# Optimization experiments

Hardware: AMD Instinct MI355X
Metric: run time of the kernel (lower is better)

Reference implementation:

```python
import jax, jax.numpy as jnp
import numpy as np
from jax import lax

EPS = 1e-5
C, H, W, G = 512, 32, 32, 32


def instance_norm(x):
    # torch InstanceNorm2d: affine=False, biased variance over (H,W)
    mu = x.mean(axis=(2, 3), keepdims=True)
    var = ((x - mu) ** 2).mean(axis=(2, 3), keepdims=True)
    return (x - mu) / jnp.sqrt(var + EPS)


def conv2d(x, w, stride=1, padding=0, groups=1, lhs_dilation=None):
    return lax.conv_general_dilated(
        x, w, (stride, stride), [(padding, padding)] * 2,
        lhs_dilation=lhs_dilation, feature_group_count=groups,
        dimension_numbers=('NCHW', 'OIHW', 'NCHW'))


def leaky_relu(x):
    return jnp.where(x >= 0, x, 0.2 * x)


def unfold(img, k, s):
    # img: (C,H,W) -> (nH*nW, C, k, k); matches torch unfold(1,k,s).unfold(2,k,s)
    c, h, w = img.shape
    nH = (h - k) // s + 1
    nW = (w - k) // s + 1
    rows = []
    for i in range(k):
        cols = [img[:, i:i + s * (nH - 1) + 1:s, j:j + s * (nW - 1) + 1:s] for j in range(k)]
        rows.append(jnp.stack(cols, axis=-1))  # (C,nH,nW,k)
    p = jnp.stack(rows, axis=-2)  # (C,nH,nW,k,k)
    return p.transpose(1, 2, 0, 3, 4).reshape(nH * nW, c, k, k)


def ral(bg, fg, rate=2, ksize=3, scale=10.0):
    # Region Affinity Layer (contextual-attention style), batch = 1
    b, c, h, w = fg.shape
    fh, fw = h // rate, w // rate
    # bilinear downsample by exactly 2 (half-pixel) == 2x2 average pooling
    fg_small = fg.reshape(b, c, fh, rate, fw, rate).mean(axis=(3, 5))
    bk = 2 * rate
    bg_patches = unfold(jnp.pad(bg, ((0, 0), (0, 0), (1, 1), (1, 1)))[0], bk, rate)      # (256,C,4,4)
    fg_patches = unfold(jnp.pad(fg_small, ((0, 0), (0, 0), (1, 1), (1, 1)))[0], ksize, 1)  # (256,C,3,3)
    norm = jnp.sqrt((fg_patches ** 2).sum(axis=(1, 2, 3), keepdims=True))
    fgp_n = fg_patches / jnp.maximum(norm, 1e-4)
    score = conv2d(fg_small, fgp_n, padding=1)        # (1,256,16,16)
    attn = jax.nn.softmax(score * scale, axis=1)
    # conv_transpose2d(attn, bg_patches, stride=rate, padding=1) via lhs dilation
    w_t = jnp.flip(bg_patches, axis=(-2, -1)).transpose(1, 0, 2, 3)  # (C,256,4,4)
    return conv2d(attn, w_t, padding=bk - 2, lhs_dilation=(rate, rate)) / 4.0  # (1,C,32,32)


def forward(x, gus, w_sk3, b_sk3, w_sk5, b_sk5, w_sk7, b_sk7,
            w_fc, b_fc, w_fc0, b_fc0, w_fc1, b_fc1, w_fc2, b_fc2, w_down, w_fuse):
    # ---- SKConv (M=3 branches: k=3/5/7, groups=32) ----
    feas = []
    for wgt, bias, pad in ((w_sk3, b_sk3, 1), (w_sk5, b_sk5, 2), (w_sk7, b_sk7, 3)):
        f = conv2d(x, wgt, padding=pad, groups=G) + bias[None, :, None, None]
        feas.append(jax.nn.relu(instance_norm(f)))
    feas = jnp.stack(feas, axis=1)                # (B,3,C,H,W)
    fea_s = feas.sum(axis=1).mean(axis=(2, 3))    # (B,C) global pool
    fea_z = fea_s @ w_fc.T + b_fc                 # (B,32)
    att = jnp.stack([fea_z @ w_fc0.T + b_fc0,
                     fea_z @ w_fc1.T + b_fc1,
                     fea_z @ w_fc2.T + b_fc2], axis=1)  # (B,3,C)
    att = jax.nn.softmax(att, axis=1)[..., None, None]
    out_32 = (feas * att).sum(axis=1)             # (1,C,32,32)
    out_res = out_32
    out_32 = ral(out_32, out_32)
    b, c, h, w = out_32.shape
    # ---- gaussian-weighted broadcast sum: (P,H,W)x(C,H,W)->(P,C)->raw reshape ----
    gus_out = jnp.einsum('pxy,cxy->pc', gus, out_32[0]).reshape(b, c, h, w)
    # ---- CSA patch correlation ----
    csa2_in = jax.nn.sigmoid(out_32)
    p_fff = unfold(jnp.pad(out_32, ((0, 0), (0, 0), (1, 1), (1, 1)))[0], 3, 1)    # (1024,C,3,3)
    p_f = unfold(jnp.pad(csa2_in, ((0, 0), (0, 0), (1, 1), (1, 1)))[0], 3, 1)     # (1024,C,3,3)
    p_conv = unfold(csa2_in[0], 1, 1)                                             # (1024,C,1,1)
    csa_a = (p_conv * p_f).mean(axis=1)                                           # (1024,3,3)
    csa_a = jax.nn.softmax(csa_a.reshape(h * w, 9), axis=1).reshape(h * w, 1, 3, 3)
    out_csa = (csa_a * p_fff).sum(axis=(-2, -1)).reshape(b, c, h, w)
    # ---- fuse ----
    z = jnp.concatenate([gus_out, out_csa], axis=1)       # (1,1024,32,32)
    z = leaky_relu(instance_norm(conv2d(z, w_down)))
    z = jnp.concatenate([z, out_res], axis=1)             # (1,1024,32,32)
    return leaky_relu(instance_norm(conv2d(z, w_fuse)))   # (1,512,32,32)


def _gaussian_buffer():
    # util.gussin(1.5): gaussian centered at every grid position of a 32x32 map
    v = 1.5
    r = np.arange(32)
    i, k, x, y = np.meshgrid(r, r, r, r, indexing='ij')
    g = np.exp(-((x - i) ** 2 + (y - k) ** 2) / (2 * v * v)) / (2 * np.pi * v * v)
    return jnp.asarray(g.reshape(32 * 32, 32, 32), dtype=jnp.float32)


def setup_inputs():
    key = jax.random.key(0)
    ks = jax.random.split(key, 12)
    s = 0.02
    return {
        'x': jax.random.normal(ks[0], (1, C, H, W), jnp.float32),
        'gus': _gaussian_buffer(),
        'w_sk3': jax.random.normal(ks[1], (C, C // G, 3, 3), jnp.float32) * s,
        'b_sk3': jnp.zeros((C,), jnp.float32),
        'w_sk5': jax.random.normal(ks[2], (C, C // G, 5, 5), jnp.float32) * s,
        'b_sk5': jnp.zeros((C,), jnp.float32),
        'w_sk7': jax.random.normal(ks[3], (C, C // G, 7, 7), jnp.float32) * s,
        'b_sk7': jnp.zeros((C,), jnp.float32),
        'w_fc': jax.random.normal(ks[4], (32, C), jnp.float32) * s,
        'b_fc': jnp.zeros((32,), jnp.float32),
        'w_fc0': jax.random.normal(ks[5], (C, 32), jnp.float32) * s,
        'b_fc0': jnp.zeros((C,), jnp.float32),
        'w_fc1': jax.random.normal(ks[6], (C, 32), jnp.float32) * s,
        'b_fc1': jnp.zeros((C,), jnp.float32),
        'w_fc2': jax.random.normal(ks[7], (C, 32), jnp.float32) * s,
        'b_fc2': jnp.zeros((C,), jnp.float32),
        'w_down': jax.random.normal(ks[8], (512, 1024, 1, 1), jnp.float32) * s,
        'w_fuse': jax.random.normal(ks[9], (512, 1024, 1, 1), jnp.float32) * s,
    }


def reference(x, gus, w_sk3, b_sk3, w_sk5, b_sk5, w_sk7, b_sk7, w_fc, b_fc,
              w_fc0, b_fc0, w_fc1, b_fc1, w_fc2, b_fc2, w_down, w_fuse):
    return forward(x, gus, w_sk3, b_sk3, w_sk5, b_sk5, w_sk7, b_sk7,
                   w_fc, b_fc, w_fc0, b_fc0, w_fc1, b_fc1, w_fc2, b_fc2,
                   w_down, w_fuse)
```

## Files before the change

kernel.cpp:

```cpp
#include <hip/hip_runtime.h>
#include <math.h>

#define EPSN 1e-5f

typedef __attribute__((ext_vector_type(8))) short bf16x8;
typedef __attribute__((ext_vector_type(4))) float f32x4;

__device__ __forceinline__ ushort f2bf(float f) {
  unsigned u = __float_as_uint(f);
  unsigned r = (u + 0x7fff + ((u >> 16) & 1)) >> 16;
  return (ushort)r;
}
__device__ __forceinline__ float bf2f(ushort h) {
  return __uint_as_float(((unsigned)h) << 16);
}

__device__ __forceinline__ void breduce2(float& a, float& b, float* lds) {
#pragma unroll
  for (int o = 32; o > 0; o >>= 1) {
    a += __shfl_down(a, o);
    b += __shfl_down(b, o);
  }
  int lane = threadIdx.x & 63, wid = threadIdx.x >> 6;
  __syncthreads();
  if (lane == 0) { lds[wid] = a; lds[4 + wid] = b; }
  __syncthreads();
  a = lds[0] + lds[1] + lds[2] + lds[3];
  b = lds[4] + lds[5] + lds[6] + lds[7];
}

__device__ __forceinline__ float breduce_sum(float v, float* lds) {
#pragma unroll
  for (int o = 32; o > 0; o >>= 1) v += __shfl_down(v, o);
  int lane = threadIdx.x & 63, wid = threadIdx.x >> 6;
  __syncthreads();
  if (lane == 0) lds[wid] = v;
  __syncthreads();
  return lds[0] + lds[1] + lds[2] + lds[3];
}

__device__ __forceinline__ float breduce_max(float v, float* lds) {
#pragma unroll
  for (int o = 32; o > 0; o >>= 1) v = fmaxf(v, __shfl_down(v, o));
  int lane = threadIdx.x & 63, wid = threadIdx.x >> 6;
  __syncthreads();
  if (lane == 0) lds[wid] = v;
  __syncthreads();
  return fmaxf(fmaxf(lds[0], lds[1]), fmaxf(lds[2], lds[3]));
}

__global__ void pre_kernel(const float* __restrict__ gus,
                           const float* __restrict__ wdown,
                           const float* __restrict__ wfuse,
                           const float* __restrict__ w3,
                           const float* __restrict__ w5,
                           const float* __restrict__ w7,
                           ushort* __restrict__ gus_bf,
                           ushort* __restrict__ wdown_bf,
                           ushort* __restrict__ wfuse_bf,
                           ushort* __restrict__ resd,
                           ushort* __restrict__ Apk_g,
                           ushort* __restrict__ Acomb,
                           float* __restrict__ diagsum) {
  int bid = blockIdx.x, tid = threadIdx.x;
  if (bid < 2048) {
    int i = bid * 1024 + tid * 4;
    if (i < 1048576) {
      float4 v = *(const float4*)&gus[i];
      int m = i >> 10, n = i & 1023;
      int y = n >> 5, x = n & 31;
      int idxb = ((y >> 1) << 4) + (x >> 1);
      int py = y & 1;
      ushort2 e0 = {f2bf(v.x), f2bf(v.z)};
      ushort2 e1 = {f2bf(v.y), f2bf(v.w)};
      *(ushort2*)&gus_bf[(size_t)m * 1024 + (py * 2 + 0) * 256 + idxb] = e0;
      *(ushort2*)&gus_bf[(size_t)m * 1024 + (py * 2 + 1) * 256 + idxb] = e1;
    } else {
      const float* src; ushort* dst; int off;
      if (i < 1572864) { src = wdown; dst = wdown_bf; off = i - 1048576; }
      else { src = wfuse; dst = wfuse_bf; off = i - 1572864; }
      float4 v = *(const float4*)&src[off];
      ushort4 o = {f2bf(v.x), f2bf(v.y), f2bf(v.z), f2bf(v.w)};
      *(ushort4*)&dst[off] = o;
    }
  } else if (bid < 2304) {
    int t8 = (bid - 2048) * 256 + tid;
    uint4 z = {0u, 0u, 0u, 0u};
#pragma unroll
    for (int k = 0; k < 4; ++k) *(uint4*)&resd[(size_t)(t8 + k * 65536) * 8] = z;
  } else if (bid < 5056) {
    int i2 = (bid - 2304) * 256 + tid;
    int g = i2 / 22016;
    int r = i2 - g * 22016;
    int p = r >> 9;
    int r5 = r & 511;
    int quad = r5 >> 7, m16 = (r5 >> 3) & 15, j = r & 7;
    int k = quad * 8 + j, tp = k >> 4, ic = k & 15;
    float val = 0.f;
    if (p < 25) {
      int t = 2 * p + tp;
      if (t < 49) val = w7[(size_t)(g * 16 + m16) * 784 + ic * 49 + t];
    } else if (p < 38) {
      int t = 2 * (p - 25) + tp;
      if (t < 25) val = w5[(size_t)(g * 16 + m16) * 400 + ic * 25 + t];
    } else {
      int t = 2 * (p - 38) + tp;
      if (t < 9) val = w3[(size_t)(g * 16 + m16) * 144 + ic * 9 + t];
    }
    Apk_g[i2] = f2bf(val);
  } else if (bid < 5568) {
    int j = (bid - 5056) * 256 + tid;
    uint4 z = {0u, 0u, 0u, 0u};
    ((uint4*)Acomb)[j] = z;
  } else {
    diagsum[tid] = 0.f;
  }
}

__global__ __launch_bounds__(256) void sk_mfma(const float* __restrict__ x,
                                               const ushort* __restrict__ Apk_g,
                                               ushort* __restrict__ feasRawH) {
  __shared__ ushort xg[10 * 38 * 24];
  int bid = blockIdx.x, tid = threadIdx.x;
  int g = bid >> 3, sl = bid & 7, y0 = sl * 4;
  for (int i = tid; i < 4560; i += 256) ((uint*)xg)[i] = 0u;
  __syncthreads();
  for (int i = tid; i < 5120; i += 256) {
    int lr = i >> 9, ic = (i >> 5) & 15, xc = i & 31;
    int y = y0 + lr - 3;
    if ((unsigned)y < 32u)
      xg[(lr * 38 + xc + 3) * 24 + ic] =
          f2bf(x[(size_t)(g * 16 + ic) * 1024 + y * 32 + xc]);
  }
  __syncthreads();
  int wv = tid >> 6, lane = tid & 63, quad = lane >> 4, m16 = lane & 15;
  int qh = (quad & 1) * 8, tp = quad >> 1;
  const ushort* Ag = Apk_g + (size_t)g * 22016;
  f32x4 acc[2][3] = {};
#pragma unroll
  for (int p = 0; p < 25; ++p) {
    bf16x8 af = *(const bf16x8*)&Ag[(p * 4 + quad) * 128 + m16 * 8];
    int t = 2 * p + tp;
    if (t > 48) t = 48;
    int ky = t / 7, kx = t - ky * 7;
#pragma unroll
    for (int ti = 0; ti < 2; ++ti) {
      int T = wv + ti * 4, tl = T >> 1, x0c = (T & 1) * 16;
      bf16x8 bf = *(const bf16x8*)&xg[((tl + ky) * 38 + x0c + m16 + kx) * 24 + qh];
      acc[ti][2] = __builtin_amdgcn_mfma_f32_16x16x32_bf16(af, bf, acc[ti][2], 0, 0, 0);
    }
  }
#pragma unroll
  for (int p = 0; p < 13; ++p) {
    bf16x8 af = *(const bf16x8*)&Ag[((p + 25) * 4 + quad) * 128 + m16 * 8];
    int t = 2 * p + tp;
    if (t > 24) t = 24;
    int ky = t / 5, kx = t - ky * 5;
#pragma unroll
    for (int ti = 0; ti < 2; ++ti) {
      int T = wv + ti * 4, tl = T >> 1, x0c = (T & 1) * 16;
      bf16x8 bf =
          *(const bf16x8*)&xg[((tl + ky + 1) * 38 + x0c + m16 + kx + 1) * 24 + qh];
      acc[ti][1] = __builtin_amdgcn_mfma_f32_16x16x32_bf16(af, bf, acc[ti][1], 0, 0, 0);
    }
  }
#pragma unroll
  for (int p = 0; p < 5; ++p) {
    bf16x8 af = *(const bf16x8*)&Ag[((p + 38) * 4 + quad) * 128 + m16 * 8];
    int t = 2 * p + tp;
    if (t > 8) t = 8;
    int ky = t / 3, kx = t - ky * 3;
#pragma unroll
    for (int ti = 0; ti < 2; ++ti) {
      int T = wv + ti * 4, tl = T >> 1, x0c = (T & 1) * 16;
      bf16x8 bf =
          *(const bf16x8*)&xg[((tl + ky + 2) * 38 + x0c + m16 + kx + 2) * 24 + qh];
      acc[ti][0] = __builtin_amdgcn_mfma_f32_16x16x32_bf16(af, bf, acc[ti][0], 0, 0, 0);
    }
  }
  int cb = g * 16 + quad * 4;
#pragma unroll
  for (int ti = 0; ti < 2; ++ti) {
    int T = wv + ti * 4, tl = T >> 1, x0c = (T & 1) * 16;
    int pos = (y0 + tl) * 32 + x0c + m16;
#pragma unroll
    for (int br = 0; br < 3; ++br)
#pragma unroll
      for (int r = 0; r < 4; ++r)
        feasRawH[(size_t)(br * 512 + cb + r) * 1024 + pos] = f2bf(acc[ti][br][r]);
  }
}

__global__ __launch_bounds__(256) void sk_norm(const ushort* __restrict__ rawH,
                                               ushort* __restrict__ feasH,
                                               float* __restrict__ bmean) {
  __shared__ float red[8];
  int mc = blockIdx.x, tid = threadIdx.x;
  float v[4];
  {
    ushort4 h = *(const ushort4*)&rawH[(size_t)mc * 1024 + tid * 4];
    v[0] = bf2f(h.x); v[1] = bf2f(h.y); v[2] = bf2f(h.z); v[3] = bf2f(h.w);
  }
  float s = 0.f, ss = 0.f;
#pragma unroll
  for (int r = 0; r < 4; ++r) { s += v[r]; ss += v[r] * v[r]; }
  breduce2(s, ss, red);
  float mean = s * (1.f / 1024.f);
  float var = ss * (1.f / 1024.f) - mean * mean;
  float inv = rsqrtf(var + EPSN);
  float rs = 0.f;
  ushort4 o;
#pragma unroll
  for (int r = 0; r < 4; ++r) {
    float t = (v[r] - mean) * inv;
    t = t > 0.f ? t : 0.f;
    ((ushort*)&o)[r] = f2bf(t);
    rs += t;
  }
  *(ushort4*)&feasH[(size_t)mc * 1024 + tid * 4] = o;
  float tot = breduce_sum(rs, red);
  if (tid == 0) bmean[mc] = tot * (1.f / 1024.f);
}

__global__ __launch_bounds__(256) void blend_fc(
    const ushort* __restrict__ feasH, const float* __restrict__ bmean,
    const float* __restrict__ wfc, const float* __restrict__ bfc,
    const float* __restrict__ w0, const float* __restrict__ b0,
    const float* __restrict__ w1, const float* __restrict__ b1,
    const float* __restrict__ w2, const float* __restrict__ b2,
    float* __restrict__ res, ushort* __restrict__ Zt2,
    ushort* __restrict__ resd) {
  __shared__ float sfea[512];
  __shared__ float zpart[8][32];
  __shared__ float zz[32];
  __shared__ float lv[3][32];
  __shared__ float attb[3][32];
  __shared__ float tile[32][33];
  int tid = threadIdx.x;
  int pb = blockIdx.x * 32, cb = blockIdx.y * 32;
  for (int c = tid; c < 512; c += 256)
    sfea[c] = bmean[c] + bmean[512 + c] + bmean[1024 + c];
  __syncthreads();
  {
    int j = tid & 31, seg = tid >> 5;
    float p = 0.f;
    for (int c = seg * 64; c < seg * 64 + 64; ++c) p += sfea[c] * wfc[j * 512 + c];
    zpart[seg][j] = p;
  }
  __syncthreads();
  if (tid < 32) {
    float d = bfc[tid];
#pragma unroll
    for (int s = 0; s < 8; ++s) d += zpart[s][tid];
    zz[tid] = d;
// ... 287 lines not shown
      a[t] = (red9[0][t] + red9[1][t] + red9[2][t] + red9[3][t]) * (1.f / 512.f);
    float mx = a[0];
#pragma unroll
    for (int t = 1; t < 9; ++t) mx = fmaxf(mx, a[t]);
    float sum = 0.f;
#pragma unroll
    for (int t = 0; t < 9; ++t) { a[t] = expf(a[t] - mx); sum += a[t]; }
    float inv = 1.f / sum;
#pragma unroll
    for (int t = 0; t < 9; ++t) a9s[t] = a[t] * inv;
  }
  __syncthreads();
  float2 acc = {0.f, 0.f};
#pragma unroll
  for (int u = 0; u < 3; ++u) {
    int yy = ny + u - 1;
#pragma unroll
    for (int v = 0; v < 3; ++v) {
      int xx = nx + v - 1;
      if ((unsigned)yy < 32u && (unsigned)xx < 32u) {
        float w = a9s[u * 3 + v];
        float2 ov = *(const float2*)&orlt[(yy * 32 + xx) * 512 + c2];
        acc.x += w * ov.x;
        acc.y += w * ov.y;
      }
    }
  }
  int kk = 512 + (n >> 1);
  int pos0 = ((n & 1) << 9) + c2;
  Zt[(size_t)pos0 * 1024 + kk] = f2bf(acc.x);
  Zt[(size_t)(pos0 + 1) * 1024 + kk] = f2bf(acc.y);
}

__global__ __launch_bounds__(256) void mfma_gemm_ks(const ushort* __restrict__ A,
                                                    const ushort* __restrict__ Bt,
                                                    float* __restrict__ Cp,
                                                    int N) {
  const int KF = 1024;
  int tid = threadIdx.x;
  int wv = tid >> 6, lane = tid & 63;
  int quad = lane >> 4, m16 = lane & 15;
  int nb = blockIdx.x * 64, mb = blockIdx.y * 64;
  int kh = blockIdx.z;
  const ushort* Ap = A + (size_t)(mb + wv * 16 + m16) * KF + kh * 512 + quad * 8;
  const ushort* Bp = Bt + (size_t)(nb + m16) * KF + kh * 512 + quad * 8;
  f32x4 ac0 = {0.f, 0.f, 0.f, 0.f}, ac1 = ac0, ac2 = ac0, ac3 = ac0;
#pragma unroll 4
  for (int k0 = 0; k0 < 512; k0 += 32) {
    bf16x8 af = *(const bf16x8*)(Ap + k0);
    bf16x8 b0 = *(const bf16x8*)(Bp + k0);
    bf16x8 b1 = *(const bf16x8*)(Bp + (size_t)16 * KF + k0);
    bf16x8 b2 = *(const bf16x8*)(Bp + (size_t)32 * KF + k0);
    bf16x8 b3 = *(const bf16x8*)(Bp + (size_t)48 * KF + k0);
    ac0 = __builtin_amdgcn_mfma_f32_16x16x32_bf16(af, b0, ac0, 0, 0, 0);
    ac1 = __builtin_amdgcn_mfma_f32_16x16x32_bf16(af, b1, ac1, 0, 0, 0);
    ac2 = __builtin_amdgcn_mfma_f32_16x16x32_bf16(af, b2, ac2, 0, 0, 0);
    ac3 = __builtin_amdgcn_mfma_f32_16x16x32_bf16(af, b3, ac3, 0, 0, 0);
  }
  int row = mb + wv * 16 + quad * 4;
  float* C = Cp + (size_t)kh * 524288;
  f32x4 accs[4] = {ac0, ac1, ac2, ac3};
#pragma unroll
  for (int nt = 0; nt < 4; ++nt)
#pragma unroll
    for (int r = 0; r < 4; ++r)
      C[(size_t)(row + r) * N + nb + nt * 16 + m16] = accs[nt][r];
}

__global__ __launch_bounds__(256) void norm_down2(const float* __restrict__ ra,
                                                  ushort* __restrict__ Zt2) {
  __shared__ float red[8];
  int c = blockIdx.x, tid = threadIdx.x;
  float v[4];
  float s = 0.f, ss = 0.f;
#pragma unroll
  for (int r = 0; r < 4; ++r) {
    int i = c * 1024 + tid + r * 256;
    v[r] = ra[i] + ra[524288 + i];
    s += v[r];
    ss += v[r] * v[r];
  }
  breduce2(s, ss, red);
  float mean = s * (1.f / 1024.f);
  float var = ss * (1.f / 1024.f) - mean * mean;
  float inv = rsqrtf(var + EPSN);
#pragma unroll
  for (int r = 0; r < 4; ++r) {
    float t = (v[r] - mean) * inv;
    t = t >= 0.f ? t : 0.2f * t;
    Zt2[(size_t)(tid + r * 256) * 1024 + c] = f2bf(t);
  }
}

__global__ __launch_bounds__(256) void norm_leaky2(const float* __restrict__ ra,
                                                   float* __restrict__ out) {
  __shared__ float red[8];
  int c = blockIdx.x, tid = threadIdx.x;
  float v[4];
  float s = 0.f, ss = 0.f;
#pragma unroll
  for (int r = 0; r < 4; ++r) {
    int i = c * 1024 + tid + r * 256;
    v[r] = ra[i] + ra[524288 + i];
    s += v[r];
    ss += v[r] * v[r];
  }
  breduce2(s, ss, red);
  float mean = s * (1.f / 1024.f);
  float var = ss * (1.f / 1024.f) - mean * mean;
  float inv = rsqrtf(var + EPSN);
#pragma unroll
  for (int r = 0; r < 4; ++r) {
    float t = (v[r] - mean) * inv;
    out[c * 1024 + tid + r * 256] = t >= 0.f ? t : 0.2f * t;
  }
}

extern "C" void kernel_launch(void* const* d_in, const int* in_sizes, int n_in,
                              void* d_out, int out_size, void* d_ws, size_t ws_size,
                              hipStream_t stream) {
  const float* x = (const float*)d_in[0];
  const float* gus = (const float*)d_in[1];
  const float* w3 = (const float*)d_in[2];
  const float* w5 = (const float*)d_in[4];
  const float* w7 = (const float*)d_in[6];
  const float* wfc = (const float*)d_in[8];
  const float* bfc = (const float*)d_in[9];
  const float* w0 = (const float*)d_in[10];
  const float* b0 = (const float*)d_in[11];
  const float* w1 = (const float*)d_in[12];
  const float* b1 = (const float*)d_in[13];
  const float* w2 = (const float*)d_in[14];
  const float* b2 = (const float*)d_in[15];
  const float* wdown = (const float*)d_in[16];
  const float* wfuse = (const float*)d_in[17];

  float* ws = (float*)d_ws;
  ushort* feasH = (ushort*)ws;
  float* rawP = ws + 786432;
  ushort* Acomb = (ushort*)rawP;
  float* bmean = ws + 1835008;
  float* res = bmean + 1536;
  float* Zt2f = res + 524288;
  ushort* Zt2 = (ushort*)Zt2f;
  float* T = Zt2f + 524288;
  ushort* feasRawH = (ushort*)T;
  float* Apart = T;
  ushort* Zt = (ushort*)T;
  float* orlt = T + 2097152;
  float* sigt = orlt + 524288;
  ushort* orlT = (ushort*)(sigt + 524288);
  ushort* gus_bf = (ushort*)(sigt + 819200);
  ushort* wdown_bf = (ushort*)(sigt + 1343488);
  ushort* wfuse_bf = (ushort*)(sigt + 1605632);
  ushort* resd = (ushort*)(sigt + 1867776);
  ushort* Apk_g = (ushort*)(sigt + 2916352);
  float* diagsum = sigt + 3268608;

  pre_kernel<<<5569, 256, 0, stream>>>(gus, wdown, wfuse, w3, w5, w7, gus_bf,
                                       wdown_bf, wfuse_bf, resd, Apk_g, Acomb,
                                       diagsum);
  sk_mfma<<<256, 256, 0, stream>>>(x, Apk_g, feasRawH);
  sk_norm<<<1536, 256, 0, stream>>>(feasRawH, feasH, bmean);
  blend_fc<<<dim3(32, 16), 256, 0, stream>>>(feasH, bmean, wfc, bfc, w0, b0, w1,
                                             b1, w2, b2, res, Zt2, resd);
  gram_part2<<<dim3(10, 1, 32), 256, 0, stream>>>(res, Apart, diagsum);
  attn_soft4<<<256, 256, 0, stream>>>(Apart, diagsum, Acomb);
  tconv2<<<dim3(16, 16), 256, 0, stream>>>(Acomb, resd, orlt, sigt, orlT);
  gus_csa<<<1152, 256, 0, stream>>>(gus_bf, orlT, sigt, orlt, Zt);
  mfma_gemm_ks<<<dim3(16, 8, 2), 256, 0, stream>>>(wdown_bf, Zt, rawP, 1024);
  norm_down2<<<512, 256, 0, stream>>>(rawP, Zt2);
  mfma_gemm_ks<<<dim3(16, 8, 2), 256, 0, stream>>>(wfuse_bf, Zt2, rawP, 1024);
  norm_leaky2<<<512, 256, 0, stream>>>(rawP, (float*)d_out);
}
```

Before: 217.5 us.

## Fuse SK weight packing and conversion prologue into conv kernel; pair-channel norm kernels

Merges the preprocessing kernel with the grouped SK conv MFMA kernel. Each conv block now packs its group's 7/5/3 weights directly into LDS, and the remaining blocks do the conversion and zeroing work, which removes one launch and the global Apk round trip. The instance-norm kernels (sk_norm, norm_down, norm_leaky) now process two channels per block with a joint four-value reduction, halving their grid sizes. In exchange, each conv block reads and repacks 22K weights on its own (eight blocks per group repeat this), and it uses about 62KB of LDS, which limits occupancy.

```diff
diff --git a/kernel.cpp b/kernel.cpp
--- a/kernel.cpp
+++ b/kernel.cpp
@@ -29,6 +29,27 @@
   b = lds[4] + lds[5] + lds[6] + lds[7];
 }
 
+__device__ __forceinline__ void breduce4(float& a, float& b, float& c, float& d,
+                                         float* lds) {
+#pragma unroll
+  for (int o = 32; o > 0; o >>= 1) {
+    a += __shfl_down(a, o);
+    b += __shfl_down(b, o);
+    c += __shfl_down(c, o);
+    d += __shfl_down(d, o);
+  }
+  int lane = threadIdx.x & 63, wid = threadIdx.x >> 6;
+  __syncthreads();
+  if (lane == 0) {
+    lds[wid] = a; lds[4 + wid] = b; lds[8 + wid] = c; lds[12 + wid] = d;
+  }
+  __syncthreads();
+  a = lds[0] + lds[1] + lds[2] + lds[3];
+  b = lds[4] + lds[5] + lds[6] + lds[7];
+  c = lds[8] + lds[9] + lds[10] + lds[11];
+  d = lds[12] + lds[13] + lds[14] + lds[15];
+}
+
 __device__ __forceinline__ float breduce_sum(float v, float* lds) {
 #pragma unroll
   for (int o = 32; o > 0; o >>= 1) v += __shfl_down(v, o);
@@ -49,79 +70,53 @@
   return fmaxf(fmaxf(lds[0], lds[1]), fmaxf(lds[2], lds[3]));
 }
 
-__global__ void pre_kernel(const float* __restrict__ gus,
-                           const float* __restrict__ wdown,
-                           const float* __restrict__ wfuse,
-                           const float* __restrict__ w3,
-                           const float* __restrict__ w5,
-                           const float* __restrict__ w7,
-                           ushort* __restrict__ gus_bf,
-                           ushort* __restrict__ wdown_bf,
-                           ushort* __restrict__ wfuse_bf,
-                           ushort* __restrict__ resd,
-                           ushort* __restrict__ Apk_g,
-                           ushort* __restrict__ Acomb,
-                           float* __restrict__ diagsum) {
+__global__ __launch_bounds__(256) void sk_pre(
+    const float* __restrict__ x, const float* __restrict__ gus,
+    const float* __restrict__ wdown, const float* __restrict__ wfuse,
+    const float* __restrict__ w3, const float* __restrict__ w5,
+    const float* __restrict__ w7,
+    ushort* __restrict__ gus_bf, ushort* __restrict__ wdown_bf,
+    ushort* __restrict__ wfuse_bf, ushort* __restrict__ resd,
+    ushort* __restrict__ AcombZ, float* __restrict__ diagsum,
+    ushort* __restrict__ feasRawH) {
   int bid = blockIdx.x, tid = threadIdx.x;
-  if (bid < 2048) {
-    int i = bid * 1024 + tid * 4;
-    if (i < 1048576) {
-      float4 v = *(const float4*)&gus[i];
-      int m = i >> 10, n = i & 1023;
-      int y = n >> 5, x = n & 31;
-      int idxb = ((y >> 1) << 4) + (x >> 1);
-      int py = y & 1;
-      ushort2 e0 = {f2bf(v.x), f2bf(v.z)};
-      ushort2 e1 = {f2bf(v.y), f2bf(v.w)};
-      *(ushort2*)&gus_bf[(size_t)m * 1024 + (py * 2 + 0) * 256 + idxb] = e0;
-      *(ushort2*)&gus_bf[(size_t)m * 1024 + (py * 2 + 1) * 256 + idxb] = e1;
+  if (bid >= 256) {
+    int vb = bid - 256;
+    if (vb < 2048) {
+      int i = vb * 1024 + tid * 4;
+      if (i < 1048576) {
+        float4 v = *(const float4*)&gus[i];
+        int m = i >> 10, n = i & 1023;
+        int y = n >> 5, xx = n & 31;
+        int idxb = ((y >> 1) << 4) + (xx >> 1);
+        int py = y & 1;
+        ushort2 e0 = {f2bf(v.x), f2bf(v.z)};
+        ushort2 e1 = {f2bf(v.y), f2bf(v.w)};
+        *(ushort2*)&gus_bf[(size_t)m * 1024 + (py * 2 + 0) * 256 + idxb] = e0;
+        *(ushort2*)&gus_bf[(size_t)m * 1024 + (py * 2 + 1) * 256 + idxb] = e1;
+      } else {
+        const float* src; ushort* dst; int off;
+        if (i < 1572864) { src = wdown; dst = wdown_bf; off = i - 1048576; }
+        else { src = wfuse; dst = wfuse_bf; off = i - 1572864; }
+        float4 v = *(const float4*)&src[off];
+        ushort4 o = {f2bf(v.x), f2bf(v.y), f2bf(v.z), f2bf(v.w)};
+        *(ushort4*)&dst[off] = o;
+      }
+    } else if (vb < 2304) {
+      if (vb == 2048) diagsum[tid] = 0.f;
+      int t8 = (vb - 2048) * 256 + tid;
+      uint4 z = {0u, 0u, 0u, 0u};
+#pragma unroll
+      for (int k = 0; k < 4; ++k) *(uint4*)&resd[(size_t)(t8 + k * 65536) * 8] = z;
     } else {
-      const float* src; ushort* dst; int off;
-      if (i < 1572864) { src = wdown; dst = wdown_bf; off = i - 1048576; }
-      else { src = wfuse; dst = wfuse_bf; off = i - 1572864; }
-      float4 v = *(const float4*)&src[off];
-      ushort4 o = {f2bf(v.x), f2bf(v.y), f2bf(v.z), f2bf(v.w)};
-      *(ushort4*)&dst[off] = o;
-    }
-  } else if (bid < 2304) {
-    int t8 = (bid - 2048) * 256 + tid;
-    uint4 z = {0u, 0u, 0u, 0u};
-#pragma unroll
-    for (int k = 0; k < 4; ++k) *(uint4*)&resd[(size_t)(t8 + k * 65536) * 8] = z;
-  } else if (bid < 5056) {
-    int i2 = (bid - 2304) * 256 + tid;
-    int g = i2 / 22016;
-    int r = i2 - g * 22016;
-    int p = r >> 9;
-    int r5 = r & 511;
-    int quad = r5 >> 7, m16 = (r5 >> 3) & 15, j = r & 7;
-    int k = quad * 8 + j, tp = k >> 4, ic = k & 15;
-    float val = 0.f;
-    if (p < 25) {
-      int t = 2 * p + tp;
-      if (t < 49) val = w7[(size_t)(g * 16 + m16) * 784 + ic * 49 + t];
-    } else if (p < 38) {
-      int t = 2 * (p - 25) + tp;
-      if (t < 25) val = w5[(size_t)(g * 16 + m16) * 400 + ic * 25 + t];
-    } else {
-      int t = 2 * (p - 38) + tp;
-      if (t < 9) val = w3[(size_t)(g * 16 + m16) * 144 + ic * 9 + t];
-    }
-    Apk_g[i2] = f2bf(val);
-  } else if (bid < 5568) {
-    int j = (bid - 5056) * 256 + tid;
-    uint4 z = {0u, 0u, 0u, 0u};
-    ((uint4*)Acomb)[j] = z;
-  } else {
-    diagsum[tid] = 0.f;
-  }
-}
-
-__global__ __launch_bounds__(256) void sk_mfma(const float* __restrict__ x,
-                                               const ushort* __restrict__ Apk_g,
-                                               ushort* __restrict__ feasRawH) {
+      int j = (vb - 2304) * 256 + tid;
+      uint4 z = {0u, 0u, 0u, 0u};
+      ((uint4*)AcombZ)[j] = z;
+    }
+    return;
+  }
+  __shared__ ushort apk[22016];
   __shared__ ushort xg[10 * 38 * 24];
-  int bid = blockIdx.x, tid = threadIdx.x;
   int g = bid >> 3, sl = bid & 7, y0 = sl * 4;
   for (int i = tid; i < 4560; i += 256) ((uint*)xg)[i] = 0u;
   __syncthreads();
@@ -132,14 +127,31 @@
       xg[(lr * 38 + xc + 3) * 24 + ic] =
           f2bf(x[(size_t)(g * 16 + ic) * 1024 + y * 32 + xc]);
   }
+  for (int i = tid; i < 22016; i += 256) {
+    int p = i >> 9;
+    int r5 = i & 511;
+    int quad = r5 >> 7, m16v = (r5 >> 3) & 15, j = i & 7;
+    int k = quad * 8 + j, tp = k >> 4, ic = k & 15;
+    float val = 0.f;
+    if (p < 25) {
+      int t = 2 * p + tp;
+      if (t < 49) val = w7[(size_t)(g * 16 + m16v) * 784 + ic * 49 + t];
+    } else if (p < 38) {
+      int t = 2 * (p - 25) + tp;
+      if (t < 25) val = w5[(size_t)(g * 16 + m16v) * 400 + ic * 25 + t];
+    } else {
+      int t = 2 * (p - 38) + tp;
+      if (t < 9) val = w3[(size_t)(g * 16 + m16v) * 144 + ic * 9 + t];
+    }
+    apk[i] = f2bf(val);
+  }
   __syncthreads();
   int wv = tid >> 6, lane = tid & 63, quad = lane >> 4, m16 = lane & 15;
   int qh = (quad & 1) * 8, tp = quad >> 1;
-  const ushort* Ag = Apk_g + (size_t)g * 22016;
   f32x4 acc[2][3] = {};
 #pragma unroll
   for (int p = 0; p < 25; ++p) {
-    bf16x8 af = *(const bf16x8*)&Ag[(p * 4 + quad) * 128 + m16 * 8];
+    bf16x8 af = *(const bf16x8*)&apk[(p * 4 + quad) * 128 + m16 * 8];
     int t = 2 * p + tp;
     if (t > 48) t = 48;
     int ky = t / 7, kx = t - ky * 7;
@@ -152,7 +164,7 @@
   }
 #pragma unroll
   for (int p = 0; p < 13; ++p) {
-    bf16x8 af = *(const bf16x8*)&Ag[((p + 25) * 4 + quad) * 128 + m16 * 8];
+    bf16x8 af = *(const bf16x8*)&apk[((p + 25) * 4 + quad) * 128 + m16 * 8];
     int t = 2 * p + tp;
     if (t > 24) t = 24;
     int ky = t / 5, kx = t - ky * 5;
@@ -166,7 +178,7 @@
   }
 #pragma unroll
   for (int p = 0; p < 5; ++p) {
-    bf16x8 af = *(const bf16x8*)&Ag[((p + 38) * 4 + quad) * 128 + m16 * 8];
+    bf16x8 af = *(const bf16x8*)&apk[((p + 38) * 4 + quad) * 128 + m16 * 8];
     int t = 2 * p + tp;
     if (t > 8) t = 8;
     int ky = t / 3, kx = t - ky * 3;
@@ -191,35 +203,50 @@
   }
 }
 
-__global__ __launch_bounds__(256) void sk_norm(const ushort* __restrict__ rawH,
-                                               ushort* __restrict__ feasH,
-                                               float* __restrict__ bmean) {
-  __shared__ float red[8];
-  int mc = blockIdx.x, tid = threadIdx.x;
-  float v[4];
+__global__ __launch_bounds__(256) void sk_norm2(const ushort* __restrict__ rawH,
+                                                ushort* __restrict__ feasH,
+                                                float* __restrict__ bmean) {
+  __shared__ float red[16];
+  int tid = threadIdx.x;
+  int mcA = blockIdx.x, mcB = mcA + 768;
+  float vA[4], vB[4];
   {
-    ushort4 h = *(const ushort4*)&rawH[(size_t)mc * 1024 + tid * 4];
-    v[0] = bf2f(h.x); v[1] = bf2f(h.y); v[2] = bf2f(h.z); v[3] = bf2f(h.w);
-  }
-  float s = 0.f, ss = 0.f;
-#pragma unroll
-  for (int r = 0; r < 4; ++r) { s += v[r]; ss += v[r] * v[r]; }
-  breduce2(s, ss, red);
-  float mean = s * (1.f / 1024.f);
-  float var = ss * (1.f / 1024.f) - mean * mean;
-  float inv = rsqrtf(var + EPSN);
-  float rs = 0.f;
-  ushort4 o;
+    ushort4 hA = *(const ushort4*)&rawH[(size_t)mcA * 1024 + tid * 4];
+    ushort4 hB = *(const ushort4*)&rawH[(size_t)mcB * 1024 + tid * 4];
+    vA[0] = bf2f(hA.x); vA[1] = bf2f(hA.y); vA[2] = bf2f(hA.z); vA[3] = bf2f(hA.w);
+    vB[0] = bf2f(hB.x); vB[1] = bf2f(hB.y); vB[2] = bf2f(hB.z); vB[3] = bf2f(hB.w);
+  }
+  float sA = 0.f, ssA = 0.f, sB = 0.f, ssB = 0.f;
 #pragma unroll
   for (int r = 0; r < 4; ++r) {
-    float t = (v[r] - mean) * inv;
-    t = t > 0.f ? t : 0.f;
-    ((ushort*)&o)[r] = f2bf(t);
-    rs += t;
-  }
-  *(ushort4*)&feasH[(size_t)mc * 1024 + tid * 4] = o;
-  float tot = breduce_sum(rs, red);
-  if (tid == 0) bmean[mc] = tot * (1.f / 1024.f);
+    sA += vA[r]; ssA += vA[r] * vA[r];
+    sB += vB[r]; ssB += vB[r] * vB[r];
+  }
+  breduce4(sA, ssA, sB, ssB, red);
+  float meanA = sA * (1.f / 1024.f);
+  float invA = rsqrtf(ssA * (1.f / 1024.f) - meanA * meanA + EPSN);
+  float meanB = sB * (1.f / 1024.f);
+  float invB = rsqrtf(ssB * (1.f / 1024.f) - meanB * meanB + EPSN);
+  float rsA = 0.f, rsB = 0.f;
+  ushort4 oA, oB;
+#pragma unroll
+  for (int r = 0; r < 4; ++r) {
+    float tA = (vA[r] - meanA) * invA;
+    tA = tA > 0.f ? tA : 0.f;
+    ((ushort*)&oA)[r] = f2bf(tA);
+    rsA += tA;
+    float tB = (vB[r] - meanB) * invB;
+    tB = tB > 0.f ? tB : 0.f;
+    ((ushort*)&oB)[r] = f2bf(tB);
+    rsB += tB;
+  }
+  *(ushort4*)&feasH[(size_t)mcA * 1024 + tid * 4] = oA;
+  *(ushort4*)&feasH[(size_t)mcB * 1024 + tid * 4] = oB;
+  breduce2(rsA, rsB, red);
+  if (tid == 0) {
+    bmean[mcA] = rsA * (1.f / 1024.f);
+    bmean[mcB] = rsB * (1.f / 1024.f);
+  }
 }
 
 __global__ __launch_bounds__(256) void blend_fc(
@@ -608,52 +635,65 @@
       C[(size_t)(row + r) * N + nb + nt * 16 + m16] = accs[nt][r];
 }
 
-__global__ __launch_bounds__(256) void norm_down2(const float* __restrict__ ra,
-                                                  ushort* __restrict__ Zt2) {
-  __shared__ float red[8];
-  int c = blockIdx.x, tid = threadIdx.x;
-  float v[4];
-  float s = 0.f, ss = 0.f;
+__global__ __launch_bounds__(256) void norm_down2p(const float* __restrict__ ra,
+                                                   ushort* __restrict__ Zt2) {
+  __shared__ float red[16];
+  int tid = threadIdx.x;
+  int c0 = blockIdx.x, c1 = c0 + 256;
+  float vA[4], vB[4];
+  float sA = 0.f, ssA = 0.f, sB = 0.f, ssB = 0.f;
 #pragma unroll
   for (int r = 0; r < 4; ++r) {
-    int i = c * 1024 + tid + r * 256;
-    v[r] = ra[i] + ra[524288 + i];
-    s += v[r];
-    ss += v[r] * v[r];
-  }
-  breduce2(s, ss, red);
-  float mean = s * (1.f / 1024.f);
-  float var = ss * (1.f / 1024.f) - mean * mean;
-  float inv = rsqrtf(var + EPSN);
+    int iA = c0 * 1024 + tid + r * 256;
+    int iB = c1 * 1024 + tid + r * 256;
+    vA[r] = ra[iA] + ra[524288 + iA];
+    vB[r] = ra[iB] + ra[524288 + iB];
+    sA += vA[r]; ssA += vA[r] * vA[r];
+    sB += vB[r]; ssB += vB[r] * vB[r];
+  }
+  breduce4(sA, ssA, sB, ssB, red);
+  float meanA = sA * (1.f / 1024.f);
+  float invA = rsqrtf(ssA * (1.f / 1024.f) - meanA * meanA + EPSN);
+  float meanB = sB * (1.f / 1024.f);
+  float invB = rsqrtf(ssB * (1.f / 1024.f) - meanB * meanB + EPSN);
 #pragma unroll
   for (int r = 0; r < 4; ++r) {
-    float t = (v[r] - mean) * inv;
-    t = t >= 0.f ? t : 0.2f * t;
-    Zt2[(size_t)(tid + r * 256) * 1024 + c] = f2bf(t);
-  }
-}
-
-__global__ __launch_bounds__(256) void norm_leaky2(const float* __restrict__ ra,
-                                                   float* __restrict__ out) {
-  __shared__ float red[8];
-  int c = blockIdx.x, tid = threadIdx.x;
-  float v[4];
-  float s = 0.f, ss = 0.f;
+    float tA = (vA[r] - meanA) * invA;
+    tA = tA >= 0.f ? tA : 0.2f * tA;
+    Zt2[(size_t)(tid + r * 256) * 1024 + c0] = f2bf(tA);
+    float tB = (vB[r] - meanB) * invB;
+    tB = tB >= 0.f ? tB : 0.2f * tB;
+    Zt2[(size_t)(tid + r * 256) * 1024 + c1] = f2bf(tB);
+  }
+}
+
+__global__ __launch_bounds__(256) void norm_leaky2p(const float* __restrict__ ra,
+                                                    float* __restrict__ out) {
+  __shared__ float red[16];
+  int tid = threadIdx.x;
+  int c0 = blockIdx.x, c1 = c0 + 256;
+  float vA[4], vB[4];
+  float sA = 0.f, ssA = 0.f, sB = 0.f, ssB = 0.f;
 #pragma unroll
   for (int r = 0; r < 4; ++r) {
-    int i = c * 1024 + tid + r * 256;
-    v[r] = ra[i] + ra[524288 + i];
-    s += v[r];
-    ss += v[r] * v[r];
-  }
-  breduce2(s, ss, red);
-  float mean = s * (1.f / 1024.f);
-  float var = ss * (1.f / 1024.f) - mean * mean;
-  float inv = rsqrtf(var + EPSN);
+    int iA = c0 * 1024 + tid + r * 256;
+    int iB = c1 * 1024 + tid + r * 256;
+    vA[r] = ra[iA] + ra[524288 + iA];
+    vB[r] = ra[iB] + ra[524288 + iB];
+    sA += vA[r]; ssA += vA[r] * vA[r];
+    sB += vB[r]; ssB += vB[r] * vB[r];
+  }
+  breduce4(sA, ssA, sB, ssB, red);
+  float meanA = sA * (1.f / 1024.f);
+  float invA = rsqrtf(ssA * (1.f / 1024.f) - meanA * meanA + EPSN);
+  float meanB = sB * (1.f / 1024.f);
+  float invB = rsqrtf(ssB * (1.f / 1024.f) - meanB * meanB + EPSN);
 #pragma unroll
   for (int r = 0; r < 4; ++r) {
-    float t = (v[r] - mean) * inv;
-    out[c * 1024 + tid + r * 256] = t >= 0.f ? t : 0.2f * t;
+    float tA = (vA[r] - meanA) * invA;
+    out[c0 * 1024 + tid + r * 256] = tA >= 0.f ? tA : 0.2f * tA;
+    float tB = (vB[r] - meanB) * invB;
+    out[c1 * 1024 + tid + r * 256] = tB >= 0.f ? tB : 0.2f * tB;
   }
 }
 
@@ -695,14 +735,12 @@
   ushort* wdown_bf = (ushort*)(sigt + 1343488);
   ushort* wfuse_bf = (ushort*)(sigt + 1605632);
   ushort* resd = (ushort*)(sigt + 1867776);
-  ushort* Apk_g = (ushort*)(sigt + 2916352);
   float* diagsum = sigt + 3268608;
 
-  pre_kernel<<<5569, 256, 0, stream>>>(gus, wdown, wfuse, w3, w5, w7, gus_bf,
-                                       wdown_bf, wfuse_bf, resd, Apk_g, Acomb,
-                                       diagsum);
-  sk_mfma<<<256, 256, 0, stream>>>(x, Apk_g, feasRawH);
-  sk_norm<<<1536, 256, 0, stream>>>(feasRawH, feasH, bmean);
+  sk_pre<<<3072, 256, 0, stream>>>(x, gus, wdown, wfuse, w3, w5, w7, gus_bf,
+                                   wdown_bf, wfuse_bf, resd, Acomb, diagsum,
+                                   feasRawH);
+  sk_norm2<<<768, 256, 0, stream>>>(feasRawH, feasH, bmean);
   blend_fc<<<dim3(32, 16), 256, 0, stream>>>(feasH, bmean, wfc, bfc, w0, b0, w1,
                                              b1, w2, b2, res, Zt2, resd);
   gram_part2<<<dim3(10, 1, 32), 256, 0, stream>>>(res, Apart, diagsum);
@@ -710,7 +748,7 @@
   tconv2<<<dim3(16, 16), 256, 0, stream>>>(Acomb, resd, orlt, sigt, orlT);
   gus_csa<<<1152, 256, 0, stream>>>(gus_bf, orlT, sigt, orlt, Zt);
   mfma_gemm_ks<<<dim3(16, 8, 2), 256, 0, stream>>>(wdown_bf, Zt, rawP, 1024);
-  norm_down2<<<512, 256, 0, stream>>>(rawP, Zt2);
+  norm_down2p<<<256, 256, 0, stream>>>(rawP, Zt2);
   mfma_gemm_ks<<<dim3(16, 8, 2), 256, 0, stream>>>(wfuse_bf, Zt2, rawP, 1024);
-  norm_leaky2<<<512, 256, 0, stream>>>(rawP, (float*)d_out);
-}
+  norm_leaky2p<<<256, 256, 0, stream>>>(rawP, (float*)d_out);
+}
```

After: 235.3 us. 8.2% more time.

## Fuse SK grouped conv MFMA with instance norm and ReLU per group

Applied to the files above, without the earlier changes.

Merges the grouped multi-kernel convolution and the following instance-norm/ReLU/mean kernel into a single kernel. Each of 32 blocks stages one whole group's input image and packed weights in LDS, then computes every branch for the full 32x32 map. Each block reduces its statistics in registers and LDS before writing normalized bf16 features and per-channel means. This removes the raw intermediate round trip through global memory and one launch. The cost is that parallelism drops from 256 blocks to 32, and each block needs a large LDS footprint.

```diff
diff --git a/kernel.cpp b/kernel.cpp
--- a/kernel.cpp
+++ b/kernel.cpp
@@ -117,109 +117,124 @@
   }
 }
 
-__global__ __launch_bounds__(256) void sk_mfma(const float* __restrict__ x,
-                                               const ushort* __restrict__ Apk_g,
-                                               ushort* __restrict__ feasRawH) {
-  __shared__ ushort xg[10 * 38 * 24];
-  int bid = blockIdx.x, tid = threadIdx.x;
-  int g = bid >> 3, sl = bid & 7, y0 = sl * 4;
-  for (int i = tid; i < 4560; i += 256) ((uint*)xg)[i] = 0u;
-  __syncthreads();
-  for (int i = tid; i < 5120; i += 256) {
-    int lr = i >> 9, ic = (i >> 5) & 15, xc = i & 31;
-    int y = y0 + lr - 3;
-    if ((unsigned)y < 32u)
-      xg[(lr * 38 + xc + 3) * 24 + ic] =
-          f2bf(x[(size_t)(g * 16 + ic) * 1024 + y * 32 + xc]);
+__global__ __launch_bounds__(256) void sk_fused(const float* __restrict__ x,
+                                                const ushort* __restrict__ Apk_g,
+                                                ushort* __restrict__ feasH,
+                                                float* __restrict__ bmean) {
+  __shared__ ushort apk[22016];
+  __shared__ ushort xg[38 * 38 * 24];
+  __shared__ float red[4][4][8];
+  int g = blockIdx.x, tid = threadIdx.x;
+  for (int i = tid; i < 17328; i += 256) ((uint*)xg)[i] = 0u;
+  {
+    const uint4* src = (const uint4*)(Apk_g + (size_t)g * 22016);
+    for (int i = tid; i < 2752; i += 256) ((uint4*)apk)[i] = src[i];
+  }
+  __syncthreads();
+  for (int i = tid; i < 16384; i += 256) {
+    int ic = i >> 10, pos = i & 1023;
+    int y = pos >> 5, xc = pos & 31;
+    xg[((y + 3) * 38 + xc + 3) * 24 + ic] =
+        f2bf(x[(size_t)(g * 16 + ic) * 1024 + pos]);
   }
   __syncthreads();
   int wv = tid >> 6, lane = tid & 63, quad = lane >> 4, m16 = lane & 15;
   int qh = (quad & 1) * 8, tp = quad >> 1;
-  const ushort* Ag = Apk_g + (size_t)g * 22016;
-  f32x4 acc[2][3] = {};
-#pragma unroll
-  for (int p = 0; p < 25; ++p) {
-    bf16x8 af = *(const bf16x8*)&Ag[(p * 4 + quad) * 128 + m16 * 8];
-    int t = 2 * p + tp;
-    if (t > 48) t = 48;
-    int ky = t / 7, kx = t - ky * 7;
+  int lanebase = m16 * 8;
+  int off16[16];
+#pragma unroll
+  for (int s = 0; s < 8; ++s)
 #pragma unroll
     for (int ti = 0; ti < 2; ++ti) {
       int T = wv + ti * 4, tl = T >> 1, x0c = (T & 1) * 16;
-      bf16x8 bf = *(const bf16x8*)&xg[((tl + ky) * 38 + x0c + m16 + kx) * 24 + qh];
-      acc[ti][2] = __builtin_amdgcn_mfma_f32_16x16x32_bf16(af, bf, acc[ti][2], 0, 0, 0);
-    }
-  }
-#pragma unroll
-  for (int p = 0; p < 13; ++p) {
-    bf16x8 af = *(const bf16x8*)&Ag[((p + 25) * 4 + quad) * 128 + m16 * 8];
-    int t = 2 * p + tp;
-    if (t > 24) t = 24;
-    int ky = t / 5, kx = t - ky * 5;
-#pragma unroll
-    for (int ti = 0; ti < 2; ++ti) {
-      int T = wv + ti * 4, tl = T >> 1, x0c = (T & 1) * 16;
-      bf16x8 bf =
-          *(const bf16x8*)&xg[((tl + ky + 1) * 38 + x0c + m16 + kx + 1) * 24 + qh];
-      acc[ti][1] = __builtin_amdgcn_mfma_f32_16x16x32_bf16(af, bf, acc[ti][1], 0, 0, 0);
-    }
-  }
-#pragma unroll
-  for (int p = 0; p < 5; ++p) {
-    bf16x8 af = *(const bf16x8*)&Ag[((p + 38) * 4 + quad) * 128 + m16 * 8];
-    int t = 2 * p + tp;
-    if (t > 8) t = 8;
-    int ky = t / 3, kx = t - ky * 3;
-#pragma unroll
-    for (int ti = 0; ti < 2; ++ti) {
-      int T = wv + ti * 4, tl = T >> 1, x0c = (T & 1) * 16;
-      bf16x8 bf =
-          *(const bf16x8*)&xg[((tl + ky + 2) * 38 + x0c + m16 + kx + 2) * 24 + qh];
-      acc[ti][0] = __builtin_amdgcn_mfma_f32_16x16x32_bf16(af, bf, acc[ti][0], 0, 0, 0);
-    }
-  }
-  int cb = g * 16 + quad * 4;
-#pragma unroll
-  for (int ti = 0; ti < 2; ++ti) {
-    int T = wv + ti * 4, tl = T >> 1, x0c = (T & 1) * 16;
-    int pos = (y0 + tl) * 32 + x0c + m16;
-#pragma unroll
-    for (int br = 0; br < 3; ++br)
-#pragma unroll
-      for (int r = 0; r < 4; ++r)
-        feasRawH[(size_t)(br * 512 + cb + r) * 1024 + pos] = f2bf(acc[ti][br][r]);
-  }
-}
-
-__global__ __launch_bounds__(256) void sk_norm(const ushort* __restrict__ rawH,
-                                               ushort* __restrict__ feasH,
-                                               float* __restrict__ bmean) {
-  __shared__ float red[8];
-  int mc = blockIdx.x, tid = threadIdx.x;
-  float v[4];
-  {
-    ushort4 h = *(const ushort4*)&rawH[(size_t)mc * 1024 + tid * 4];
-    v[0] = bf2f(h.x); v[1] = bf2f(h.y); v[2] = bf2f(h.z); v[3] = bf2f(h.w);
-  }
-  float s = 0.f, ss = 0.f;
-#pragma unroll
-  for (int r = 0; r < 4; ++r) { s += v[r]; ss += v[r] * v[r]; }
-  breduce2(s, ss, red);
-  float mean = s * (1.f / 1024.f);
-  float var = ss * (1.f / 1024.f) - mean * mean;
-  float inv = rsqrtf(var + EPSN);
-  float rs = 0.f;
-  ushort4 o;
-#pragma unroll
-  for (int r = 0; r < 4; ++r) {
-    float t = (v[r] - mean) * inv;
-    t = t > 0.f ? t : 0.f;
-    ((ushort*)&o)[r] = f2bf(t);
-    rs += t;
-  }
-  *(ushort4*)&feasH[(size_t)mc * 1024 + tid * 4] = o;
-  float tot = breduce_sum(rs, red);
-  if (tid == 0) bmean[mc] = tot * (1.f / 1024.f);
+      off16[s * 2 + ti] = ((s * 4 + tl) * 38 + x0c + m16) * 24 + qh;
+    }
+
+#define SK_BRANCH(NP, POFF, KS, TMAX, SHIFT, BR)                               \
+  {                                                                            \
+    f32x4 acc[16] = {};                                                        \
+    for (int p = 0; p < NP; ++p) {                                             \
+      bf16x8 af = *(const bf16x8*)&apk[((p + POFF) * 4 + quad) * 128 + lanebase]; \
+      int t = 2 * p + tp;                                                      \
+      if (t > TMAX) t = TMAX;                                                  \
+      int ky = t / KS, kx = t - ky * KS;                                       \
+      int base = (ky * 38 + kx + SHIFT * 39) * 24;                             \
+      _Pragma("unroll")                                                        \
+      for (int u = 0; u < 16; ++u) {                                           \
+        bf16x8 bf = *(const bf16x8*)&xg[off16[u] + base];                      \
+        acc[u] = __builtin_amdgcn_mfma_f32_16x16x32_bf16(af, bf, acc[u], 0, 0, 0); \
+      }                                                                        \
+    }                                                                          \
+            \
+    float s4[4] = {0.f, 0.f, 0.f, 0.f}, ss4[4] = {0.f, 0.f, 0.f, 0.f};         \
+    _Pragma("unroll")                                                          \
+    for (int u = 0; u < 16; ++u)                                               \
+      _Pragma("unroll")                                                        \
+      for (int r = 0; r < 4; ++r) {                                            \
+        float v = acc[u][r];                                                   \
+        s4[r] += v;                                                            \
+        ss4[r] += v * v;                                                       \
+      }                                                                        \
+    _Pragma("unroll")                                                          \
+    for (int o = 8; o > 0; o >>= 1)                                            \
+      _Pragma("unroll")                                                        \
+      for (int r = 0; r < 4; ++r) {                                            \
+        s4[r] += __shfl_xor(s4[r], o);                                         \
+        ss4[r] += __shfl_xor(ss4[r], o);                                       \
+      }                                                                        \
+    if (m16 == 0)                                                              \
+      _Pragma("unroll")                                                        \
+      for (int r = 0; r < 4; ++r) {                                            \
+        red[wv][quad][r] = s4[r];                                              \
+        red[wv][quad][4 + r] = ss4[r];                                         \
+      }                                                                        \
+    __syncthreads();                                                           \
+    float mean[4], inv[4];                                                     \
+    _Pragma("unroll")                                                          \
+    for (int r = 0; r < 4; ++r) {                                              \
+      float S = red[0][quad][r] + red[1][quad][r] + red[2][quad][r] +          \
+                red[3][quad][r];                                               \
+      float SS = red[0][quad][4 + r] + red[1][quad][4 + r] +                   \
+                 red[2][quad][4 + r] + red[3][quad][4 + r];                    \
+      mean[r] = S * (1.f / 1024.f);                                            \
+      inv[r] = rsqrtf(SS * (1.f / 1024.f) - mean[r] * mean[r] + EPSN);         \
+    }                                                                          \
+    float rs[4] = {0.f, 0.f, 0.f, 0.f};                                        \
+    _Pragma("unroll")                                                          \
+    for (int u = 0; u < 16; ++u) {                                             \
+      int T = wv + (u & 1) * 4, tl = T >> 1, x0c = (T & 1) * 16;               \
+      int pos = ((u >> 1) * 4 + tl) * 32 + x0c + m16;                          \
+      _Pragma("unroll")                                                        \
+      for (int r = 0; r < 4; ++r) {                                            \
+        float tv = (acc[u][r] - mean[r]) * inv[r];                             \
+        tv = tv > 0.f ? tv : 0.f;                                              \
+        feasH[(size_t)(BR * 512 + g * 16 + quad * 4 + r) * 1024 + pos] =       \
+            f2bf(tv);                                                          \
+        rs[r] += tv;                                                           \
+      }                                                                        \
+    }                                                                          \
+    _Pragma("unroll")                                                          \
+    for (int o = 8; o > 0; o >>= 1)                                            \
+      _Pragma("unroll")                                                        \
+      for (int r = 0; r < 4; ++r) rs[r] += __shfl_xor(rs[r], o);               \
+    __syncthreads();                                                           \
+    if (m16 == 0)                                                              \
+      _Pragma("unroll")                                                        \
+      for (int r = 0; r < 4; ++r) red[wv][quad][r] = rs[r];                    \
+    __syncthreads();                                                           \
+    if (wv == 0 && m16 == 0)                                                   \
+      _Pragma("unroll")                                                        \
+      for (int r = 0; r < 4; ++r)                                              \
+        bmean[BR * 512 + g * 16 + quad * 4 + r] =                              \
+            (red[0][quad][r] + red[1][quad][r] + red[2][quad][r] +             \
+             red[3][quad][r]) * (1.f / 1024.f);                                \
+    __syncthreads();                                                           \
+  }
+
+  SK_BRANCH(25, 0, 7, 48, 0, 2)
+  SK_BRANCH(13, 25, 5, 24, 1, 1)
+  SK_BRANCH(5, 38, 3, 8, 2, 0)
+#undef SK_BRANCH
 }
 
 __global__ __launch_bounds__(256) void blend_fc(
@@ -685,7 +700,6 @@
   float* Zt2f = res + 524288;
   ushort* Zt2 = (ushort*)Zt2f;
   float* T = Zt2f + 524288;
-  ushort* feasRawH = (ushort*)T;
   float* Apart = T;
   ushort* Zt = (ushort*)T;
   float* orlt = T + 2097152;
@@ -701,8 +715,7 @@
   pre_kernel<<<5569, 256, 0, stream>>>(gus, wdown, wfuse, w3, w5, w7, gus_bf,
                                        wdown_bf, wfuse_bf, resd, Apk_g, Acomb,
                                        diagsum);
-  sk_mfma<<<256, 256, 0, stream>>>(x, Apk_g, feasRawH);
-  sk_norm<<<1536, 256, 0, stream>>>(feasRawH, feasH, bmean);
+  sk_fused<<<32, 256, 0, stream>>>(x, Apk_g, feasH, bmean);
   blend_fc<<<dim3(32, 16), 256, 0, stream>>>(feasH, bmean, wfc, bfc, w0, b0, w1,
                                              b1, w2, b2, res, Zt2, resd);
   gram_part2<<<dim3(10, 1, 32), 256, 0, stream>>>(res, Apart, diagsum);
```

Result: slower. 235.4 us (+8.3%).

## Drop split-K in 1x1 GEMMs and scatter SK weight packing by source index

Applied to the files above, without the earlier changes.

The two 1x1-conv GEMMs no longer split K into two halves with partial fp32 outputs. Each block now covers the full K with a 32-wide N tile, and the norm kernels read a single result instead of summing two partials. The SK weight packing in the pre-kernel now reads w7/w5/w3 coalesced and scatters into the packed layout, with one block zeroing the padding slots, instead of gathering per packed element. This removes the partial-sum traffic and the scattered weight reads, at the cost of longer K loops per block and scattered bf16 writes.

```diff
diff --git a/kernel.cpp b/kernel.cpp
--- a/kernel.cpp
+++ b/kernel.cpp
@@ -88,32 +88,47 @@
     uint4 z = {0u, 0u, 0u, 0u};
 #pragma unroll
     for (int k = 0; k < 4; ++k) *(uint4*)&resd[(size_t)(t8 + k * 65536) * 8] = z;
-  } else if (bid < 5056) {
-    int i2 = (bid - 2304) * 256 + tid;
-    int g = i2 / 22016;
-    int r = i2 - g * 22016;
-    int p = r >> 9;
-    int r5 = r & 511;
-    int quad = r5 >> 7, m16 = (r5 >> 3) & 15, j = r & 7;
-    int k = quad * 8 + j, tp = k >> 4, ic = k & 15;
-    float val = 0.f;
-    if (p < 25) {
-      int t = 2 * p + tp;
-      if (t < 49) val = w7[(size_t)(g * 16 + m16) * 784 + ic * 49 + t];
-    } else if (p < 38) {
-      int t = 2 * (p - 25) + tp;
-      if (t < 25) val = w5[(size_t)(g * 16 + m16) * 400 + ic * 25 + t];
-    } else {
-      int t = 2 * (p - 38) + tp;
-      if (t < 9) val = w3[(size_t)(g * 16 + m16) * 144 + ic * 9 + t];
-    }
-    Apk_g[i2] = f2bf(val);
-  } else if (bid < 5568) {
-    int j = (bid - 5056) * 256 + tid;
+  } else if (bid < 2816) {
+    int j = (bid - 2304) * 256 + tid;
     uint4 z = {0u, 0u, 0u, 0u};
     ((uint4*)Acomb)[j] = z;
+  } else if (bid == 2816) {
+    diagsum[tid] = 0.f;
+    const int PV[3] = {24, 37, 42};
+    for (int i = tid; i < 24576; i += 256) {
+      int g = i / 768, rr = i - g * 768;
+      int which = rr >> 8, r2 = rr & 255;
+      int quad = 2 + (r2 >> 7), m16 = (r2 >> 3) & 15, j = r2 & 7;
+      Apk_g[(size_t)g * 22016 + (PV[which] * 4 + quad) * 128 + m16 * 8 + j] = 0;
+    }
   } else {
-    diagsum[tid] = 0.f;
+    int v = (bid - 2817) * 256 + tid;
+    int oc, ic, t, p;
+    float val;
+    if (v < 401408) {
+      int s = v;
+      oc = s / 784; int rem = s - oc * 784;
+      ic = rem / 49; t = rem - ic * 49;
+      p = (t >> 1);
+      val = w7[s];
+    } else if (v < 606208) {
+      int s = v - 401408;
+      oc = s / 400; int rem = s - oc * 400;
+      ic = rem / 25; t = rem - ic * 25;
+      p = (t >> 1) + 25;
+      val = w5[s];
+    } else {
+      int s = v - 606208;
+      oc = s / 144; int rem = s - oc * 144;
+      ic = rem / 9; t = rem - ic * 9;
+      p = (t >> 1) + 38;
+      val = w3[s];
+    }
+    int tp = t & 1;
+    int k = tp * 16 + ic;
+    int quad = k >> 3, j = k & 7;
+    Apk_g[(size_t)(oc >> 4) * 22016 + (p * 4 + quad) * 128 + (oc & 15) * 8 + j] =
+        f2bf(val);
   }
 }
 
@@ -573,39 +588,32 @@
   Zt[(size_t)(pos0 + 1) * 1024 + kk] = f2bf(acc.y);
 }
 
-__global__ __launch_bounds__(256) void mfma_gemm_ks(const ushort* __restrict__ A,
-                                                    const ushort* __restrict__ Bt,
-                                                    float* __restrict__ Cp,
-                                                    int N) {
+__global__ __launch_bounds__(256) void mfma_gemm_n(const ushort* __restrict__ A,
+                                                   const ushort* __restrict__ Bt,
+                                                   float* __restrict__ C) {
   const int KF = 1024;
   int tid = threadIdx.x;
   int wv = tid >> 6, lane = tid & 63;
   int quad = lane >> 4, m16 = lane & 15;
-  int nb = blockIdx.x * 64, mb = blockIdx.y * 64;
-  int kh = blockIdx.z;
-  const ushort* Ap = A + (size_t)(mb + wv * 16 + m16) * KF + kh * 512 + quad * 8;
-  const ushort* Bp = Bt + (size_t)(nb + m16) * KF + kh * 512 + quad * 8;
-  f32x4 ac0 = {0.f, 0.f, 0.f, 0.f}, ac1 = ac0, ac2 = ac0, ac3 = ac0;
+  int nb = blockIdx.x * 32, mb = blockIdx.y * 64;
+  const ushort* Ap = A + (size_t)(mb + wv * 16 + m16) * KF + quad * 8;
+  const ushort* Bp = Bt + (size_t)(nb + m16) * KF + quad * 8;
+  f32x4 ac0 = {0.f, 0.f, 0.f, 0.f}, ac1 = ac0;
 #pragma unroll 4
-  for (int k0 = 0; k0 < 512; k0 += 32) {
+  for (int k0 = 0; k0 < KF; k0 += 32) {
     bf16x8 af = *(const bf16x8*)(Ap + k0);
     bf16x8 b0 = *(const bf16x8*)(Bp + k0);
     bf16x8 b1 = *(const bf16x8*)(Bp + (size_t)16 * KF + k0);
-    bf16x8 b2 = *(const bf16x8*)(Bp + (size_t)32 * KF + k0);
-    bf16x8 b3 = *(const bf16x8*)(Bp + (size_t)48 * KF + k0);
     ac0 = __builtin_amdgcn_mfma_f32_16x16x32_bf16(af, b0, ac0, 0, 0, 0);
     ac1 = __builtin_amdgcn_mfma_f32_16x16x32_bf16(af, b1, ac1, 0, 0, 0);
-    ac2 = __builtin_amdgcn_mfma_f32_16x16x32_bf16(af, b2, ac2, 0, 0, 0);
-    ac3 = __builtin_amdgcn_mfma_f32_16x16x32_bf16(af, b3, ac3, 0, 0, 0);
   }
   int row = mb + wv * 16 + quad * 4;
-  float* C = Cp + (size_t)kh * 524288;
-  f32x4 accs[4] = {ac0, ac1, ac2, ac3};
-#pragma unroll
-  for (int nt = 0; nt < 4; ++nt)
+  f32x4 accs[2] = {ac0, ac1};
+#pragma unroll
+  for (int nt = 0; nt < 2; ++nt)
 #pragma unroll
     for (int r = 0; r < 4; ++r)
-      C[(size_t)(row + r) * N + nb + nt * 16 + m16] = accs[nt][r];
+      C[(size_t)(row + r) * 1024 + nb + nt * 16 + m16] = accs[nt][r];
 }
 
 __global__ __launch_bounds__(256) void norm_down2(const float* __restrict__ ra,
@@ -616,8 +624,7 @@
   float s = 0.f, ss = 0.f;
 #pragma unroll
   for (int r = 0; r < 4; ++r) {
-    int i = c * 1024 + tid + r * 256;
-    v[r] = ra[i] + ra[524288 + i];
+    v[r] = ra[c * 1024 + tid + r * 256];
     s += v[r];
     ss += v[r] * v[r];
   }
@@ -641,8 +648,7 @@
   float s = 0.f, ss = 0.f;
 #pragma unroll
   for (int r = 0; r < 4; ++r) {
-    int i = c * 1024 + tid + r * 256;
-    v[r] = ra[i] + ra[524288 + i];
+    v[r] = ra[c * 1024 + tid + r * 256];
     s += v[r];
     ss += v[r] * v[r];
   }
@@ -698,7 +704,7 @@
   ushort* Apk_g = (ushort*)(sigt + 2916352);
   float* diagsum = sigt + 3268608;
 
-  pre_kernel<<<5569, 256, 0, stream>>>(gus, wdown, wfuse, w3, w5, w7, gus_bf,
+  pre_kernel<<<5473, 256, 0, stream>>>(gus, wdown, wfuse, w3, w5, w7, gus_bf,
                                        wdown_bf, wfuse_bf, resd, Apk_g, Acomb,
                                        diagsum);
   sk_mfma<<<256, 256, 0, stream>>>(x, Apk_g, feasRawH);
@@ -709,8 +715,8 @@
   attn_soft4<<<256, 256, 0, stream>>>(Apart, diagsum, Acomb);
   tconv2<<<dim3(16, 16), 256, 0, stream>>>(Acomb, resd, orlt, sigt, orlT);
   gus_csa<<<1152, 256, 0, stream>>>(gus_bf, orlT, sigt, orlt, Zt);
-  mfma_gemm_ks<<<dim3(16, 8, 2), 256, 0, stream>>>(wdown_bf, Zt, rawP, 1024);
+  mfma_gemm_n<<<dim3(32, 8), 256, 0, stream>>>(wdown_bf, Zt, rawP);
   norm_down2<<<512, 256, 0, stream>>>(rawP, Zt2);
-  mfma_gemm_ks<<<dim3(16, 8, 2), 256, 0, stream>>>(wfuse_bf, Zt2, rawP, 1024);
+  mfma_gemm_n<<<dim3(32, 8), 256, 0, stream>>>(wfuse_bf, Zt2, rawP);
   norm_leaky2<<<512, 256, 0, stream>>>(rawP, (float*)d_out);
 }
```

Result: slower. 227.4 us (+4.6%).
